# Kernel tuning notes

Hardware: AMD Instinct MI355X
Metric: run time of the kernel (lower is better)

The kernel has to match this reference:

```python
import jax, jax.numpy as jnp
import numpy as np

N = 8192
INP_DIM = 512
OUT_DIM = 256


def setup_inputs() -> dict:
    key = jax.random.key(0)
    k1, k2, k3, k4, k5 = jax.random.split(key, 5)
    x = jax.random.normal(k1, (N, INP_DIM), dtype=jnp.float32)
    adj = jax.random.uniform(k2, (N, N), dtype=jnp.float32)  # threshold at 0.5 below
    # learned params: w ~ torch.rand(inp_dim, out_dim); Linear(out_dim, out_dim)
    w = jax.random.uniform(k3, (INP_DIM, OUT_DIM), dtype=jnp.float32)
    bound = 1.0 / np.sqrt(OUT_DIM)
    lin_w = jax.random.uniform(k4, (OUT_DIM, OUT_DIM), minval=-bound, maxval=bound, dtype=jnp.float32)
    lin_b = jax.random.uniform(k5, (OUT_DIM,), minval=-bound, maxval=bound, dtype=jnp.float32)
    return {"x": x, "adj": adj, "w": w, "lin_w": lin_w, "lin_b": lin_b}


def reference(x, adj, w, lin_w, lin_b):
    n = adj.shape[0]
    # A = binarize(adj) + I
    A = jnp.where(adj > 0.5, 1.0, 0.0) + jnp.eye(n, dtype=adj.dtype)
    # D is diagonal, so inverse().sqrt() == diag(1/sqrt(deg)); deg >= 1 from self-loops
    d_inv_sqrt = jax.lax.rsqrt(jnp.sum(A, axis=1))  # [N]
    # A_hat = D^{-1/2} A D^{-1/2} as row/col scaling (same math, O(N^2))
    A_hat = A * d_inv_sqrt[:, None] * d_inv_sqrt[None, :]
    # message passing + feature transform
    h = jax.nn.relu((A_hat @ x) @ w)           # [N, out_dim]
    return h @ lin_w.T + lin_b                  # Linear(out_dim, out_dim)
```

## Files before the change

### kernel.cpp

```cpp
#include <hip/hip_runtime.h>
#include <hip/hip_bf16.h>

typedef __attribute__((ext_vector_type(4))) float f32x4;
typedef __attribute__((ext_vector_type(8))) short s16x8;
typedef unsigned int uint;
typedef unsigned short ushort;
typedef unsigned long long u64;


__device__ inline ushort f2bf(float f) {
  union { float f; uint u; } v; v.f = f;
  uint r = (v.u + 0x7FFFu + ((v.u >> 16) & 1u)) >> 16;
  return (ushort)r;
}
__device__ inline float bf2f(ushort h) { union { uint u; float f; } v; v.u = ((uint)h) << 16; return v.f; }
__device__ inline uint pack2(float a, float b) { return (uint)f2bf(a) | ((uint)f2bf(b) << 16); }
__device__ inline int kappa(int j) {
  return (j & ~255) | ((j & 3) << 6) | (((j >> 7) & 1) << 5) | ((j >> 2) & 31);
}
__device__ inline int ikappa(int k) {
  return (k & ~255) | ((k >> 6) & 3) | (((k >> 5) & 1) << 7) | ((k & 31) << 2);
}

__global__ __launch_bounds__(256, 4) void k_pack(const float* __restrict__ adj,
                                                 const float* __restrict__ w,
                                                 const float* __restrict__ lw,
                                                 uint* __restrict__ bits,
                                                 float* __restrict__ dinv,
                                                 float* __restrict__ dk,
                                                 ushort* __restrict__ wT,
                                                 ushort* __restrict__ lwb) {
  const int t = threadIdx.x, lane = t & 63, wv = t >> 6;
  const int b = blockIdx.x;
  const int row = b * 4 + wv;
  const float4* src = (const float4*)(adj + (size_t)row * 8192) + lane;
  uint* dst = bits + (size_t)row * 256;
  float4 A[4], B[4], C[4];
#pragma unroll
  for (int j = 0; j < 4; ++j) A[j] = src[j * 64];
#pragma unroll
  for (int j = 0; j < 4; ++j) B[j] = src[256 + j * 64];
  int cnt = 0;
#pragma unroll
  for (int bt = 0; bt < 8; ++bt) {
    if (bt + 2 < 8) {
#pragma unroll
      for (int j = 0; j < 4; ++j) C[j] = src[(bt + 2) * 256 + j * 64];
    }
#pragma unroll
    for (int j = 0; j < 4; ++j) {
      u64 b0 = __ballot(A[j].x > 0.5f), b1 = __ballot(A[j].y > 0.5f);
      u64 b2 = __ballot(A[j].z > 0.5f), b3 = __ballot(A[j].w > 0.5f);
      cnt += __popcll(b0) + __popcll(b1) + __popcll(b2) + __popcll(b3);
      if ((lane & 31) == 0) {
        uint4 v = (lane == 0)
          ? make_uint4((uint)b0, (uint)(b0 >> 32), (uint)b1, (uint)(b1 >> 32))
          : make_uint4((uint)b2, (uint)(b2 >> 32), (uint)b3, (uint)(b3 >> 32));
        *(uint4*)(dst + (bt * 4 + j) * 8 + (lane >> 5) * 4) = v;
      }
    }
#pragma unroll
    for (int j = 0; j < 4; ++j) { A[j] = B[j]; B[j] = C[j]; }
  }
  if (lane == 0) {
    float d = rsqrtf((float)(cnt + 1));
    dinv[row] = d;
    dk[kappa(row)] = d;
  }
  if (b < 16) {
#pragma unroll
    for (int kk = 0; kk < 32; ++kk) {
      int k = b * 32 + kk;
      wT[(size_t)t * 512 + k] = f2bf(w[(size_t)k * 256 + t]);
    }
  } else if (b < 24) {
    const int b2 = b - 16;
    const float4* s = (const float4*)lw + b2 * 2048;
    uint2* d = (uint2*)lwb + b2 * 2048;
#pragma unroll
    for (int ii = 0; ii < 8; ++ii) {
      float4 v = s[ii * 256 + t];
      uint2 p; p.x = pack2(v.x, v.y); p.y = pack2(v.z, v.w);
      d[ii * 256 + t] = p;
    }
  }
}

__global__ __launch_bounds__(512) void k_xw(const float* __restrict__ x,
                                            const ushort* __restrict__ wT,
                                            const float* __restrict__ dk,
                                            ushort* __restrict__ PB,
                                            ushort* __restrict__ zRow) {
  __shared__ ushort xa[2][32 * 64];
  const int b = blockIdx.x;
  const int bp = (b & 7) * 32 + (b >> 3);
  const int t = threadIdx.x;
  const int lane = t & 63, wid = t >> 6;
  const int mg = wid >> 2, ng = wid & 3;
  const int rl = lane & 15, kg = lane >> 4;
  const int srow = t >> 4, sseg = t & 15;
  const int jrow = ((bp >> 3) << 8) + ((bp & 1) << 7) + ((bp >> 1) & 3) + srow * 4;
  const float4* xsrc = (const float4*)(x + (size_t)jrow * 512) + sseg;
  const int swb = (sseg * 8) ^ ((srow & 7) << 4);
  const int arow = mg * 16 + rl;
  float4 xv[8];
#pragma unroll
  for (int kc2 = 0; kc2 < 8; kc2++) xv[kc2] = xsrc[kc2 * 16];

  f32x4 acc[4];
#pragma unroll
  for (int q = 0; q < 4; q++) acc[q] = (f32x4){0.f, 0.f, 0.f, 0.f};

  {
    uint2 pk; pk.x = pack2(xv[0].x, xv[0].y); pk.y = pack2(xv[0].z, xv[0].w);
    *(uint2*)((char*)xa[0] + srow * 128 + swb) = pk;
  }
#pragma unroll
  for (int kc2 = 0; kc2 < 8; kc2++) {
    __syncthreads();
    if (kc2 < 7) {
      uint2 pk; pk.x = pack2(xv[kc2 + 1].x, xv[kc2 + 1].y);
      pk.y = pack2(xv[kc2 + 1].z, xv[kc2 + 1].w);
      *(uint2*)((char*)xa[(kc2 + 1) & 1] + srow * 128 + swb) = pk;
    }
#pragma unroll
    for (int ks = 0; ks < 2; ks++) {
      union { uint4 u; s16x8 s; } av;
      av.u = *(uint4*)((char*)xa[kc2 & 1] + arow * 128 + ((ks * 64 + kg * 16) ^ ((rl & 7) << 4)));
#pragma unroll
      for (int q = 0; q < 4; q++) {
        int n = ng * 64 + q * 16 + rl;
        union { uint4 u; s16x8 s; } bv;
        bv.u = *(const uint4*)(wT + (size_t)n * 512 + kc2 * 64 + ks * 32 + kg * 8);
        acc[q] = __builtin_amdgcn_mfma_f32_16x16x32_bf16(av.s, bv.s, acc[q], 0, 0, 0);
      }
    }
  }
  const int kb = bp * 32 + mg * 16 + kg * 4;
  float4 dk4 = *(const float4*)(dk + kb);
  const float dkv[4] = {dk4.x, dk4.y, dk4.z, dk4.w};
  char* pb0 = (char*)PB + (size_t)bp * 16384 + (mg * 2 + (kg >> 1)) * 256 + rl * 16 + (kg & 1) * 8;
#pragma unroll
  for (int q = 0; q < 4; q++) {
    int n = ng * 64 + q * 16 + rl;
    ushort zu[4];
#pragma unroll
    for (int r = 0; r < 4; r++) zu[r] = f2bf(acc[q][r] * dkv[r]);
    uint2 p;
    p.x = (uint)zu[0] | ((uint)zu[1] << 16);
    p.y = (uint)zu[2] | ((uint)zu[3] << 16);
    *(uint2*)(pb0 + (ng * 4 + q) * 1024) = p;
#pragma unroll
    for (int r = 0; r < 4; r++)
      zRow[(size_t)ikappa(kb + r) * 256 + n] = zu[r];
  }
}

__global__ __launch_bounds__(512) void k_spmm(const uint* __restrict__ bits,
                                              const ushort* __restrict__ PB,
                                              ushort* __restrict__ part) {
  __shared__ uint4 blds4[256 * 8];
  __shared__ uint2 lut[16];
  const int bx = blockIdx.x;
  const int kc = bx & 7, mb = bx >> 3;
  const int m0 = mb * 256;
  const int t = threadIdx.x;
  const int lane = t & 63, wid = t >> 6;
  const int mg = wid >> 2, ng = wid & 3;
  const int rl = lane & 15, kg = lane >> 4;
  if (t < 16) {
    uint2 e;
    e.x = ((t & 1u) ? 0x3F80u : 0u) | ((t & 2u) ? 0x3F800000u : 0u);
    e.y = ((t & 4u) ? 0x3F80u : 0u) | ((t & 8u) ? 0x3F800000u : 0u);
    lut[t] = e;
  }
  {
    const int r = t >> 1, h = t & 1;
    const uint4* src = (const uint4*)(bits + (size_t)(m0 + r) * 256 + kc * 32 + h * 16);
#pragma unroll
    for (int i = 0; i < 4; ++i)
      blds4[r * 8 + ((h * 4 + i) ^ (r & 7))] = src[i];
  }
  const char* zb0 = (const char*)PB + (size_t)kc * 32 * 16384 + ng * 4096 + kg * 256 + rl * 16;
  __syncthreads();

  uint4 bufA[4], bufB[4];
#pragma unroll
  for (int q = 0; q < 4; ++q) bufA[q] = *(const uint4*)(zb0 + q * 1024);

  f32x4 acc[8][4];
#pragma unroll
  for (int f = 0; f < 8; ++f)
#pragma unroll
    for (int q = 0; q < 4; ++q) acc[f][q] = (f32x4){0.f, 0.f, 0.f, 0.f};

  int abase[8];
#pragma unroll
  for (int f = 0; f < 8; ++f) abase[f] = (mg * 128 + f * 16 + rl) * 8;
  const int axor = rl & 7;
  const uint shft = kg * 8;

  for (int a = 0; a < 8; ++a) {
    uint4 aw[8];
#pragma unroll
    for (int f = 0; f < 8; ++f) aw[f] = blds4[abase[f] + (a ^ axor)];
#pragma unroll
    for (int s = 0; s < 4; ++s) {
      const int ks = a * 4 + s;
      const uint4* use = (s & 1) ? bufB : bufA;
      uint4* nxt = (s & 1) ? bufA : bufB;
      if (ks < 31) {
#pragma unroll
        for (int q = 0; q < 4; ++q)
          nxt[q] = *(const uint4*)(zb0 + (size_t)(ks + 1) * 16384 + q * 1024);
      }
#pragma unroll
      for (int f = 0; f < 8; ++f) {
        uint wrd = (s == 0) ? aw[f].x : (s == 1) ? aw[f].y : (s == 2) ? aw[f].z : aw[f].w;
        uint byt = (wrd >> shft) & 0xFFu;
        uint2 lo = lut[byt & 0xFu];
        uint2 hi = lut[byt >> 4];
        union { uint4 u; s16x8 s8; } au;
        au.u = make_uint4(lo.x, lo.y, hi.x, hi.y);
#pragma unroll
        for (int q = 0; q < 4; ++q) {
          union { uint4 u; s16x8 s8; } bu; bu.u = use[q];
          acc[f][q] = __builtin_amdgcn_mfma_f32_16x16x32_bf16(au.s8, bu.s8, acc[f][q], 0, 0, 0);
        }
      }
    }
  }
  ushort* pb = part + ((size_t)kc << 21);
#pragma unroll
  for (int f = 0; f < 8; ++f)
#pragma unroll
    for (int q = 0; q < 4; ++q) {
      int n = ng * 64 + q * 16 + rl;
      int mm = m0 + mg * 128 + f * 16 + kg * 4;
      uint2 p;
      p.x = pack2(acc[f][q][0], acc[f][q][1]);
      p.y = pack2(acc[f][q][2], acc[f][q][3]);
      *(uint2*)(pb + (size_t)n * 8192 + mm) = p;
    }
}

__global__ __launch_bounds__(512) void k_lin(const ushort* __restrict__ part,
                                             const ushort* __restrict__ zRow,
                                             const float* __restrict__ dinv,
                                             const ushort* __restrict__ lwb,
                                             const float* __restrict__ lb,
                                             float* __restrict__ out) {
  __shared__ ushort hA[32 * 256];
  __shared__ float sdinv[32];
  const int m0 = blockIdx.x * 32;
  const int t = threadIdx.x;
  if (t < 32) sdinv[t] = dinv[m0 + t];
  {
    const int n = t >> 1, mh = t & 1;
    float sum[16];
#pragma unroll
    for (int j = 0; j < 16; ++j)
      sum[j] = bf2f(zRow[(size_t)(m0 + mh * 16 + j) * 256 + n]);
#pragma unroll
    for (int kcp = 0; kcp < 8; kcp++) {
      const ushort* pp = part + (size_t)kcp * 2097152 + (size_t)n * 8192 + m0 + mh * 16;
      uint4 pa = *(const uint4*)pp, pbq = *(const uint4*)(pp + 8);
      uint pu[8] = {pa.x, pa.y, pa.z, pa.w, pbq.x, pbq.y, pbq.z, pbq.w};
#pragma unroll
      for (int i = 0; i < 8; i++) {
        sum[2 * i]     += bf2f((ushort)(pu[i] & 0xFFFF));
        sum[2 * i + 1] += bf2f((ushort)(pu[i] >> 16));
      }
    }
    __syncthreads();
#pragma unroll
    for (int j = 0; j < 16; j++) {
      int m = mh * 16 + j;
      float h = sum[j] * sdinv[m];
      h = h > 0.f ? h : 0.f;
      *(ushort*)((char*)hA + m * 512 + ((n * 2) ^ ((m & 7) << 4))) = f2bf(h);
    }
  }
  __syncthreads();
  const int lane = t & 63, wid = t >> 6;
  const int rl = lane & 15, kg = lane >> 4;
  f32x4 acc[2][2];
#pragma unroll
  for (int f = 0; f < 2; f++)
#pragma unroll
    for (int q = 0; q < 2; q++) acc[f][q] = (f32x4){0.f, 0.f, 0.f, 0.f};

#pragma unroll
  for (int ks = 0; ks < 8; ks++) {
    union { uint4 u; s16x8 s; } av[2];
#pragma unroll
    for (int f = 0; f < 2; f++)
      av[f].u = *(uint4*)((char*)hA + (f * 16 + rl) * 512 + ((ks * 64 + kg * 16) ^ ((rl & 7) << 4)));
#pragma unroll
    for (int q = 0; q < 2; q++) {
      int no = wid * 32 + q * 16 + rl;
      union { uint4 u; s16x8 s; } bv;
      bv.u = *(const uint4*)(lwb + (size_t)no * 256 + ks * 32 + kg * 8);
#pragma unroll
      for (int f = 0; f < 2; f++)
        acc[f][q] = __builtin_amdgcn_mfma_f32_16x16x32_bf16(av[f].s, bv.s, acc[f][q], 0, 0, 0);
    }
  }
#pragma unroll
  for (int q = 0; q < 2; q++) {
    int no = wid * 32 + q * 16 + rl;
    float bb = lb[no];
#pragma unroll
    for (int f = 0; f < 2; f++) {
      int mbase = m0 + f * 16 + kg * 4;
#pragma unroll
      for (int r = 0; r < 4; r++)
        out[(size_t)(mbase + r) * 256 + no] = acc[f][q][r] + bb;
    }
  }
}

extern "C" void kernel_launch(void* const* d_in, const int* in_sizes, int n_in,
                              void* d_out, int out_size, void* d_ws, size_t ws_size,
                              hipStream_t stream) {
  const float* x   = (const float*)d_in[0];
  const float* adj = (const float*)d_in[1];
  const float* w   = (const float*)d_in[2];
  const float* lw  = (const float*)d_in[3];
  const float* lb  = (const float*)d_in[4];
  float* out = (float*)d_out;

  char* ws = (char*)d_ws;
  float*  dinv = (float*)(ws + 0);
  float*  dk   = (float*)(ws + (32u << 10));
  ushort* lwb  = (ushort*)(ws + (128u << 10));
  ushort* wT   = (ushort*)(ws + (256u << 10));
  uint*   bits = (uint*)(ws + (1ull << 20));
  ushort* PB   = (ushort*)(ws + (9ull << 20));
  ushort* part = (ushort*)(ws + (16ull << 20));
  ushort* zRow = (ushort*)(ws + (48ull << 20));

  hipLaunchKernelGGL(k_pack, dim3(2048), dim3(256), 0, stream, adj, w, lw, bits, dinv, dk, wT, lwb);
  hipLaunchKernelGGL(k_xw, dim3(256), dim3(512), 0, stream, x, wT, dk, PB, zRow);
  hipLaunchKernelGGL(k_spmm, dim3(256), dim3(512), 0, stream, bits, PB, part);
  hipLaunchKernelGGL(k_lin, dim3(256), dim3(512), 0, stream, part, zRow, dinv, lwb, lb, out);
}
```

Measured before the change: 130.4 us.

## Retile spmm to 128-row by 4-way K split, tile partial layout, stage zRow stores

The SpMM kernel now splits K 4 ways instead of 8, with 128-row blocks instead of 256, using a 16-wide swizzle for the bit tile. Each block reads twice as much PB and does half as many partial sums. Partials go into a blocked layout (m-tile, kc, n, 32) so k_lin can read them contiguously with fewer passes. k_xw stages its zRow output through shared memory to make coalesced 16-byte stores instead of scattered 2-byte stores. The block-to-tile mapping is also changed to match the new K split. The trade-off is more B traffic per spmm block, which lowers reuse of the A tile.

```diff
diff --git a/kernel.cpp b/kernel.cpp
--- a/kernel.cpp
+++ b/kernel.cpp
@@ -92,8 +92,9 @@
                                             ushort* __restrict__ PB,
                                             ushort* __restrict__ zRow) {
   __shared__ ushort xa[2][32 * 64];
+  __shared__ ushort zs[32 * 264];
   const int b = blockIdx.x;
-  const int bp = (b & 7) * 32 + (b >> 3);
+  const int bp = (b & 3) * 64 + (b >> 2);
   const int t = threadIdx.x;
   const int lane = t & 63, wid = t >> 6;
   const int mg = wid >> 2, ng = wid & 3;
@@ -140,6 +141,7 @@
   float4 dk4 = *(const float4*)(dk + kb);
   const float dkv[4] = {dk4.x, dk4.y, dk4.z, dk4.w};
   char* pb0 = (char*)PB + (size_t)bp * 16384 + (mg * 2 + (kg >> 1)) * 256 + rl * 16 + (kg & 1) * 8;
+  const int kk0 = mg * 16 + kg * 4;
 #pragma unroll
   for (int q = 0; q < 4; q++) {
     int n = ng * 64 + q * 16 + rl;
@@ -151,19 +153,27 @@
     p.y = (uint)zu[2] | ((uint)zu[3] << 16);
     *(uint2*)(pb0 + (ng * 4 + q) * 1024) = p;
 #pragma unroll
-    for (int r = 0; r < 4; r++)
-      zRow[(size_t)ikappa(kb + r) * 256 + n] = zu[r];
+    for (int r = 0; r < 4; r++) zs[(kk0 + r) * 264 + n] = zu[r];
+  }
+  __syncthreads();
+  {
+    const int rr = t >> 4, seg = t & 15;
+    uint4 v0 = *(uint4*)&zs[rr * 264 + seg * 16];
+    uint4 v1 = *(uint4*)&zs[rr * 264 + seg * 16 + 8];
+    ushort* dst = zRow + (size_t)ikappa(bp * 32 + rr) * 256 + seg * 16;
+    *(uint4*)dst = v0;
+    *(uint4*)(dst + 8) = v1;
   }
 }
 
 __global__ __launch_bounds__(512) void k_spmm(const uint* __restrict__ bits,
                                               const ushort* __restrict__ PB,
-                                              ushort* __restrict__ part) {
-  __shared__ uint4 blds4[256 * 8];
+                                              ushort* __restrict__ part2) {
+  __shared__ uint4 blds4[128 * 16];
   __shared__ uint2 lut[16];
   const int bx = blockIdx.x;
-  const int kc = bx & 7, mb = bx >> 3;
-  const int m0 = mb * 256;
+  const int kc = bx & 3, mb = bx >> 2;
+  const int m0 = mb * 128;
   const int t = threadIdx.x;
   const int lane = t & 63, wid = t >> 6;
   const int mg = wid >> 2, ng = wid & 3;
@@ -175,47 +185,49 @@
     lut[t] = e;
   }
   {
-    const int r = t >> 1, h = t & 1;
-    const uint4* src = (const uint4*)(bits + (size_t)(m0 + r) * 256 + kc * 32 + h * 16);
-#pragma unroll
-    for (int i = 0; i < 4; ++i)
-      blds4[r * 8 + ((h * 4 + i) ^ (r & 7))] = src[i];
-  }
-  const char* zb0 = (const char*)PB + (size_t)kc * 32 * 16384 + ng * 4096 + kg * 256 + rl * 16;
+    const int r = t >> 2, p = t & 3;
+    const uint4* src = (const uint4*)(bits + (size_t)(m0 + r) * 256 + kc * 64);
+#pragma unroll
+    for (int i = 0; i < 4; ++i) {
+      int g = p * 4 + i;
+      blds4[r * 16 + (g ^ (r & 15))] = src[g];
+    }
+  }
+  const char* zb0 = (const char*)PB + (size_t)kc * 64 * 16384 + ng * 4096 + kg * 256 + rl * 16;
   __syncthreads();
 
   uint4 bufA[4], bufB[4];
 #pragma unroll
   for (int q = 0; q < 4; ++q) bufA[q] = *(const uint4*)(zb0 + q * 1024);
 
-  f32x4 acc[8][4];
-#pragma unroll
-  for (int f = 0; f < 8; ++f)
+  f32x4 acc[4][4];
+#pragma unroll
+  for (int f = 0; f < 4; ++f)
 #pragma unroll
     for (int q = 0; q < 4; ++q) acc[f][q] = (f32x4){0.f, 0.f, 0.f, 0.f};
 
-  int abase[8];
-#pragma unroll
-  for (int f = 0; f < 8; ++f) abase[f] = (mg * 128 + f * 16 + rl) * 8;
-  const int axor = rl & 7;
+  int abase[4];
+#pragma unroll
+  for (int f = 0; f < 4; ++f) abase[f] = (mg * 64 + f * 16 + rl) * 16;
+  const int axor = rl;
   const uint shft = kg * 8;
 
-  for (int a = 0; a < 8; ++a) {
-    uint4 aw[8];
-#pragma unroll
-    for (int f = 0; f < 8; ++f) aw[f] = blds4[abase[f] + (a ^ axor)];
+  for (int a = 0; a < 16; ++a) {
+    uint4 aw[4];
+#pragma unroll
+    for (int f = 0; f < 4; ++f) aw[f] = blds4[abase[f] + (a ^ axor)];
 #pragma unroll
     for (int s = 0; s < 4; ++s) {
       const int ks = a * 4 + s;
       const uint4* use = (s & 1) ? bufB : bufA;
       uint4* nxt = (s & 1) ? bufA : bufB;
-      if (ks < 31) {
+      if (ks < 63) {
 #pragma unroll
         for (int q = 0; q < 4; ++q)
           nxt[q] = *(const uint4*)(zb0 + (size_t)(ks + 1) * 16384 + q * 1024);
       }
 #pragma unroll
-      for (int f = 0; f < 8; ++f) {
+      for (int f = 0; f < 4; ++f) {
         uint wrd = (s == 0) ? aw[f].x : (s == 1) ? aw[f].y : (s == 2) ? aw[f].z : aw[f].w;
         uint byt = (wrd >> shft) & 0xFFu;
         uint2 lo = lut[byt & 0xFu];
@@ -230,21 +242,21 @@
       }
     }
   }
-  ushort* pb = part + ((size_t)kc << 21);
-#pragma unroll
-  for (int f = 0; f < 8; ++f)
+#pragma unroll
+  for (int f = 0; f < 4; ++f)
 #pragma unroll
     for (int q = 0; q < 4; ++q) {
       int n = ng * 64 + q * 16 + rl;
-      int mm = m0 + mg * 128 + f * 16 + kg * 4;
+      int mt = mb * 4 + mg * 2 + (f >> 1);
+      int moff = (f & 1) * 16 + kg * 4;
       uint2 p;
       p.x = pack2(acc[f][q][0], acc[f][q][1]);
       p.y = pack2(acc[f][q][2], acc[f][q][3]);
-      *(uint2*)(pb + (size_t)n * 8192 + mm) = p;
-    }
-}
-
-__global__ __launch_bounds__(512) void k_lin(const ushort* __restrict__ part,
+      *(uint2*)(part2 + ((((size_t)mt * 4 + kc) * 256 + n) * 32 + moff)) = p;
+    }
+}
+
+__global__ __launch_bounds__(512) void k_lin(const ushort* __restrict__ part2,
                                              const ushort* __restrict__ zRow,
                                              const float* __restrict__ dinv,
                                              const ushort* __restrict__ lwb,
@@ -256,14 +268,14 @@
   const int t = threadIdx.x;
   if (t < 32) sdinv[t] = dinv[m0 + t];
   {
-    const int n = t >> 1, mh = t & 1;
+    const int n = t & 255, mh = t >> 8;
     float sum[16];
 #pragma unroll
     for (int j = 0; j < 16; ++j)
       sum[j] = bf2f(zRow[(size_t)(m0 + mh * 16 + j) * 256 + n]);
 #pragma unroll
-    for (int kcp = 0; kcp < 8; kcp++) {
-      const ushort* pp = part + (size_t)kcp * 2097152 + (size_t)n * 8192 + m0 + mh * 16;
+    for (int kcp = 0; kcp < 4; kcp++) {
+      const ushort* pp = part2 + (((size_t)blockIdx.x * 4 + kcp) * 256 + n) * 32 + mh * 16;
       uint4 pa = *(const uint4*)pp, pbq = *(const uint4*)(pp + 8);
       uint pu[8] = {pa.x, pa.y, pa.z, pa.w, pbq.x, pbq.y, pbq.z, pbq.w};
 #pragma unroll
@@ -331,17 +343,17 @@
   float* out = (float*)d_out;
 
   char* ws = (char*)d_ws;
-  float*  dinv = (float*)(ws + 0);
-  float*  dk   = (float*)(ws + (32u << 10));
-  ushort* lwb  = (ushort*)(ws + (128u << 10));
-  ushort* wT   = (ushort*)(ws + (256u << 10));
-  uint*   bits = (uint*)(ws + (1ull << 20));
-  ushort* PB   = (ushort*)(ws + (9ull << 20));
-  ushort* part = (ushort*)(ws + (16ull << 20));
-  ushort* zRow = (ushort*)(ws + (48ull << 20));
+  float*  dinv  = (float*)(ws + 0);
+  float*  dk    = (float*)(ws + (32u << 10));
+  ushort* lwb   = (ushort*)(ws + (128u << 10));
+  ushort* wT    = (ushort*)(ws + (256u << 10));
+  uint*   bits  = (uint*)(ws + (1ull << 20));
+  ushort* PB    = (ushort*)(ws + (9ull << 20));
+  ushort* part2 = (ushort*)(ws + (16ull << 20));
+  ushort* zRow  = (ushort*)(ws + (48ull << 20));
 
   hipLaunchKernelGGL(k_pack, dim3(2048), dim3(256), 0, stream, adj, w, lw, bits, dinv, dk, wT, lwb);
   hipLaunchKernelGGL(k_xw, dim3(256), dim3(512), 0, stream, x, wT, dk, PB, zRow);
-  hipLaunchKernelGGL(k_spmm, dim3(256), dim3(512), 0, stream, bits, PB, part);
-  hipLaunchKernelGGL(k_lin, dim3(256), dim3(512), 0, stream, part, zRow, dinv, lwb, lb, out);
-}
+  hipLaunchKernelGGL(k_spmm, dim3(256), dim3(512), 0, stream, bits, PB, part2);
+  hipLaunchKernelGGL(k_lin, dim3(256), dim3(512), 0, stream, part2, zRow, dinv, lwb, lb, out);
+}
```

New measurement: 120.6 us. 1.08x faster.
